# Performance work log

Hardware: AMD Instinct MI355X
Metric: run time of the kernel (lower is better)

Reference implementation:

```python
import jax, jax.numpy as jnp
import numpy as np

H = 1024          # hidden_size
V = 50257         # output_size (vocab)
L = 64            # max_length


def setup_inputs() -> dict:
    key = jax.random.key(0)
    ks = jax.random.split(key, 20)
    s = 0.02
    inp = {
        "input": jax.random.randint(ks[0], (1,), 0, V, dtype=jnp.int64) if jax.config.jax_enable_x64 else jax.random.randint(ks[0], (1,), 0, V, dtype=jnp.int32),
        "hidden": jax.random.normal(ks[1], (2, 1, H), dtype=jnp.float32),
        "encoder_output": jax.random.normal(ks[2], (1, 2 * H), dtype=jnp.float32),
        "encoder_outputs": jax.random.normal(ks[3], (L, 2 * H), dtype=jnp.float32),
        # parameters
        "emb": jax.random.normal(ks[4], (V, H), dtype=jnp.float32) * s,
        "attn_W": jax.random.normal(ks[5], (L, 3 * H), dtype=jnp.float32) * s,
        "attn_b": jnp.zeros((L,), dtype=jnp.float32),
        "comb_W": jax.random.normal(ks[6], (H, 3 * H), dtype=jnp.float32) * s,
        "comb_b": jnp.zeros((H,), dtype=jnp.float32),
        "Wih_f": jax.random.normal(ks[7], (3 * H, H), dtype=jnp.float32) * s,
        "Whh_f": jax.random.normal(ks[8], (3 * H, H), dtype=jnp.float32) * s,
        "bih_f": jnp.zeros((3 * H,), dtype=jnp.float32),
        "bhh_f": jnp.zeros((3 * H,), dtype=jnp.float32),
        "Wih_b": jax.random.normal(ks[9], (3 * H, H), dtype=jnp.float32) * s,
        "Whh_b": jax.random.normal(ks[10], (3 * H, H), dtype=jnp.float32) * s,
        "bih_b": jnp.zeros((3 * H,), dtype=jnp.float32),
        "bhh_b": jnp.zeros((3 * H,), dtype=jnp.float32),
        "out_W": jax.random.normal(ks[11], (V, 2 * H), dtype=jnp.float32) * s,
        "out_b": jnp.zeros((V,), dtype=jnp.float32),
    }
    return inp


def _gru_cell(x, h, Wih, Whh, bih, bhh):
    # PyTorch GRUCell gate math; x, h: (1, H)
    gi = x @ Wih.T + bih                      # (1, 3H)
    gh = h @ Whh.T + bhh                      # (1, 3H)
    ir, iz, inn = jnp.split(gi, 3, axis=1)
    hr, hz, hn = jnp.split(gh, 3, axis=1)
    r = jax.nn.sigmoid(ir + hr)
    z = jax.nn.sigmoid(iz + hz)
    n = jnp.tanh(inn + r * hn)
    return (1.0 - z) * n + z * h


def reference(input, hidden, encoder_output, encoder_outputs,
              emb, attn_W, attn_b, comb_W, comb_b,
              Wih_f, Whh_f, bih_f, bhh_f,
              Wih_b, Whh_b, bih_b, bhh_b,
              out_W, out_b):
    embedded = emb[input]                     # (1, H); dropout is identity in eval
    h0, h1 = hidden[0], hidden[1]             # (1, H) each
    cat3 = jnp.concatenate([embedded, h0, h1], axis=1)          # (1, 3H)
    attn_weights = jax.nn.softmax(cat3 @ attn_W.T + attn_b, axis=1)  # (1, L)
    attn_applied = attn_weights @ encoder_outputs               # (1, 2H)
    comb = jnp.concatenate([embedded, attn_applied], axis=1)    # (1, 3H)
    x = jax.nn.relu(comb @ comb_W.T + comb_b)                   # (1, H)
    hf = _gru_cell(x, h0, Wih_f, Whh_f, bih_f, bhh_f)           # forward dir
    hb = _gru_cell(x, h1, Wih_b, Whh_b, bih_b, bhh_b)           # backward dir (seq_len=1)
    gru_out = jnp.concatenate([hf, hb], axis=1)                 # (1, 2H)
    new_hidden = jnp.stack([hf, hb], axis=0)                    # (2, 1, H)
    log_probs = jax.nn.log_softmax(gru_out @ out_W.T + out_b, axis=1)  # (1, V)
    return (log_probs, new_hidden, attn_weights)
```

## Files before the change

### kernel.cpp

```cpp
#include <hip/hip_runtime.h>
#include <hip/hip_bf16.h>
#include <math.h>

#define H   1024
#define V   50257
#define L   64
#define H2  2048
#define H3  3072

typedef float float4v __attribute__((ext_vector_type(4)));

#define WS_ATTN_LOGITS 0
#define WS_AA          128
#define WS_X           2176
#define WS_GRU         3200
#define WS_LOGITS      5248
#define WS_RED         55552

#define GEMV_BLOCKS 1024
#define GEMV_WAVES  (GEMV_BLOCKS * 4)
#define VC          20480

__device__ inline float waveReduceSum(float v) {
#pragma unroll
    for (int off = 32; off > 0; off >>= 1) v += __shfl_down(v, off, 64);
    return v;
}
__device__ inline float waveAllMax(float v) {
#pragma unroll
    for (int off = 32; off > 0; off >>= 1) v = fmaxf(v, __shfl_xor(v, off, 64));
    return v;
}
__device__ inline float waveAllSum(float v) {
#pragma unroll
    for (int off = 32; off > 0; off >>= 1) v += __shfl_xor(v, off, 64);
    return v;
}
__device__ inline void lse_combine(float& m, float& s, float m2, float s2) {
    float M = fmaxf(m, m2);
    s = s * expf(m - M) + s2 * expf(m2 - M);
    m = M;
}

__global__ __launch_bounds__(256) void k_attn_logits(
        const int* __restrict__ tok_p, const float* __restrict__ hidden,
        const float* __restrict__ emb, const float* __restrict__ attn_W,
        const float* __restrict__ attn_b, float* __restrict__ ws) {
    int b = blockIdx.x;
    int tid = threadIdx.x;
    int tok = tok_p[0];
    const float4* w4   = (const float4*)(attn_W + (size_t)b * H3);
    const float4* emb4 = (const float4*)(emb + (size_t)tok * H);
    const float4* hid4 = (const float4*)hidden;
    float acc = 0.f;
#pragma unroll
    for (int k = 0; k < 3; ++k) {
        int idx = tid + k * 256;
        float4 c = (idx < 256) ? emb4[idx] : hid4[idx - 256];
        float4 w = w4[idx];
        acc += c.x * w.x + c.y * w.y + c.z * w.z + c.w * w.w;
    }
    __shared__ float red[4];
    float p = waveReduceSum(acc);
    int lane = tid & 63, wid = tid >> 6;
    if (lane == 0) red[wid] = p;
    __syncthreads();
    if (tid == 0) ws[WS_ATTN_LOGITS + b] = red[0] + red[1] + red[2] + red[3] + attn_b[b];
}

__global__ __launch_bounds__(256) void k_softmax_applied(
        const float* __restrict__ eo, float* __restrict__ ws,
        float* __restrict__ d_out) {
    __shared__ float aw[64];
    int tid = threadIdx.x;
    if (tid < 64) {
        float x = ws[WS_ATTN_LOGITS + tid];
        float m = waveAllMax(x);
        float e = expf(x - m);
        float s = waveAllSum(e);
        float w = e / s;
        aw[tid] = w;
        if (blockIdx.x == 0) d_out[V + H2 + tid] = w;
    }
    __syncthreads();
    int j = blockIdx.x * 256 + tid;
    float acc = 0.f;
#pragma unroll 8
    for (int l = 0; l < L; ++l) acc += aw[l] * eo[l * H2 + j];
    ws[WS_AA + j] = acc;
}

__global__ __launch_bounds__(256) void k_comb_relu(
        const int* __restrict__ tok_p, const float* __restrict__ emb,
        const float* __restrict__ comb_W, const float* __restrict__ comb_b,
        float* __restrict__ ws) {
    int tid = threadIdx.x;
    int lane = tid & 63, wid = tid >> 6;
    int r = blockIdx.x * 4 + wid;
    int tok = tok_p[0];
    const float4* emb4 = (const float4*)(emb + (size_t)tok * H);
    const float4* aa4  = (const float4*)(ws + WS_AA);
    const float4v* w4  = (const float4v*)(comb_W + (size_t)r * H3);
    float acc = 0.f;
#pragma unroll
    for (int k = 0; k < 12; ++k) {
        int idx = lane + k * 64;
        float4 c = (idx < 256) ? emb4[idx] : aa4[idx - 256];
        float4v w = __builtin_nontemporal_load(&w4[idx]);
        acc += c.x * w.x + c.y * w.y + c.z * w.z + c.w * w.w;
    }
    acc = waveReduceSum(acc);
    if (lane == 0) ws[WS_X + r] = fmaxf(acc + comb_b[r], 0.f);
}

__global__ __launch_bounds__(256) void k_gru(
        const float* __restrict__ hidden,
        const float* __restrict__ Wih_f, const float* __restrict__ Whh_f,
        const float* __restrict__ bih_f, const float* __restrict__ bhh_f,
        const float* __restrict__ Wih_b, const float* __restrict__ Whh_b,
        const float* __restrict__ bih_b, const float* __restrict__ bhh_b,
        float* __restrict__ d_out, float* __restrict__ ws) {
    int tid = threadIdx.x;
    int lane = tid & 63, wid = tid >> 6;
    int w = blockIdx.x * 4 + wid;
    int dir = w >> 10;
    int i = w & (H - 1);
    const float* Wih = dir ? Wih_b : Wih_f;
    const float* Whh = dir ? Whh_b : Whh_f;
    const float* bih = dir ? bih_b : bih_f;
    const float* bhh = dir ? bhh_b : bhh_f;
    const float* h = hidden + dir * H;
    const float4* x4  = (const float4*)(ws + WS_X);
    const float4* h4  = (const float4*)h;
    const float4v* wi0 = (const float4v*)(Wih + (size_t)i * H);
    const float4v* wi1 = (const float4v*)(Wih + (size_t)(H + i) * H);
    const float4v* wi2 = (const float4v*)(Wih + (size_t)(2 * H + i) * H);
    const float4v* wh0 = (const float4v*)(Whh + (size_t)i * H);
    const float4v* wh1 = (const float4v*)(Whh + (size_t)(H + i) * H);
    const float4v* wh2 = (const float4v*)(Whh + (size_t)(2 * H + i) * H);
    float a0 = 0, a1 = 0, a2 = 0, b0 = 0, b1 = 0, b2 = 0;
#pragma unroll
    for (int k = 0; k < 4; ++k) {
        int idx = lane + k * 64;
        float4 xv = x4[idx], hv = h4[idx];
        float4v u0 = __builtin_nontemporal_load(&wi0[idx]);
        float4v u1 = __builtin_nontemporal_load(&wi1[idx]);
        float4v u2 = __builtin_nontemporal_load(&wi2[idx]);
        float4v v0 = __builtin_nontemporal_load(&wh0[idx]);
        float4v v1 = __builtin_nontemporal_load(&wh1[idx]);
        float4v v2 = __builtin_nontemporal_load(&wh2[idx]);
        a0 += xv.x*u0.x + xv.y*u0.y + xv.z*u0.z + xv.w*u0.w;
        a1 += xv.x*u1.x + xv.y*u1.y + xv.z*u1.z + xv.w*u1.w;
        a2 += xv.x*u2.x + xv.y*u2.y + xv.z*u2.z + xv.w*u2.w;
        b0 += hv.x*v0.x + hv.y*v0.y + hv.z*v0.z + hv.w*v0.w;
        b1 += hv.x*v1.x + hv.y*v1.y + hv.z*v1.z + hv.w*v1.w;
        b2 += hv.x*v2.x + hv.y*v2.y + hv.z*v2.z + hv.w*v2.w;
    }
    a0 = waveReduceSum(a0); a1 = waveReduceSum(a1); a2 = waveReduceSum(a2);
    b0 = waveReduceSum(b0); b1 = waveReduceSum(b1); b2 = waveReduceSum(b2);
    if (lane == 0) {
        float ir = a0 + bih[i],     iz = a1 + bih[H + i], in_ = a2 + bih[2 * H + i];
        float hr = b0 + bhh[i],     hz = b1 + bhh[H + i], hn  = b2 + bhh[2 * H + i];
        float r = 1.f / (1.f + expf(-(ir + hr)));
        float z = 1.f / (1.f + expf(-(iz + hz)));
        float n = tanhf(in_ + r * hn);
        float hv = (1.f - z) * n + z * h[i];
        d_out[V + dir * H + i] = hv;
        ws[WS_GRU + dir * H + i] = hv;
    }
}

template <bool NT>
__device__ inline float dot_row(const float4v* __restrict__ w4,
                                const float4 g[8], int lane) {
    float acc = 0.f;
#pragma unroll
    for (int k = 0; k < 8; ++k) {
        int idx = lane + k * 64;
        float4v w = NT ? __builtin_nontemporal_load(&w4[idx]) : w4[idx];
        acc += g[k].x * w.x + g[k].y * w.y + g[k].z * w.z + g[k].w * w.w;
    }
    return acc;
}

__global__ __launch_bounds__(256) void k_gemv_lse(
        const float* __restrict__ out_W, const float* __restrict__ out_b,
        float* __restrict__ ws) {
    int tid = threadIdx.x;
    int lane = tid & 63, wid = tid >> 6;
    int gw = blockIdx.x * 4 + wid;
    const float4* g4 = (const float4*)(ws + WS_GRU);
    float4 g[8];
#pragma unroll
    for (int k = 0; k < 8; ++k) g[k] = g4[lane + k * 64];
    float m = -3.0e38f, s = 0.f;
    for (int v = gw; v < V; v += 2 * GEMV_WAVES) {
        int v2 = v + GEMV_WAVES;
        const float4v* w0 = (const float4v*)(out_W + (size_t)v * H2);
        float acc0, acc1 = 0.f;
        acc0 = (v < VC) ? dot_row<false>(w0, g, lane)
                        : dot_row<true >(w0, g, lane);
        if (v2 < V) {
            const float4v* w1 = (const float4v*)(out_W + (size_t)v2 * H2);
            acc1 = (v2 < VC) ? dot_row<false>(w1, g, lane)
                             : dot_row<true >(w1, g, lane);
        }
        acc0 = waveReduceSum(acc0);
        acc1 = waveReduceSum(acc1);
        if (lane == 0) {
            float logit = acc0 + out_b[v];
            ws[WS_LOGITS + v] = logit;
            float M = fmaxf(m, logit);
            s = s * expf(m - M) + expf(logit - M);
            m = M;
            if (v2 < V) {
                float logit2 = acc1 + out_b[v2];
                ws[WS_LOGITS + v2] = logit2;
                M = fmaxf(m, logit2);
                s = s * expf(m - M) + expf(logit2 - M);
                m = M;
            }
        }
    }
    __shared__ float mm[4], ss[4];
    if (lane == 0) { mm[wid] = m; ss[wid] = s; }
    __syncthreads();
    if (tid == 0) {
        float M = mm[0], S = ss[0];
        lse_combine(M, S, mm[1], ss[1]);
        lse_combine(M, S, mm[2], ss[2]);
        lse_combine(M, S, mm[3], ss[3]);
        ws[WS_RED + 2 * blockIdx.x]     = M;
        ws[WS_RED + 2 * blockIdx.x + 1] = S;
    }
}

__global__ __launch_bounds__(256) void k_lse_sub(const float* __restrict__ ws,
                                                 float* __restrict__ d_out) {
    int tid = threadIdx.x;
    int lane = tid & 63, wid = tid >> 6;
    float m = -3.0e38f, s = 0.f;
#pragma unroll
    for (int k = 0; k < 4; ++k) {
        int i = tid + k * 256;
        lse_combine(m, s, ws[WS_RED + 2 * i], ws[WS_RED + 2 * i + 1]);
    }
#pragma unroll
    for (int off = 32; off > 0; off >>= 1) {
        float m2 = __shfl_xor(m, off, 64);
        float s2 = __shfl_xor(s, off, 64);
        lse_combine(m, s, m2, s2);
    }
    __shared__ float mm[4], ss[4], Csh;
    if (lane == 0) { mm[wid] = m; ss[wid] = s; }
    __syncthreads();
    if (tid == 0) {
        float M = mm[0], S = ss[0];
        lse_combine(M, S, mm[1], ss[1]);
        lse_combine(M, S, mm[2], ss[2]);
        lse_combine(M, S, mm[3], ss[3]);
        Csh = M + logf(S);
    }
    __syncthreads();
    float C = Csh;
    int v = blockIdx.x * 256 + tid;
    if (v < V) d_out[v] = ws[WS_LOGITS + v] - C;
}

extern "C" void kernel_launch(void* const* d_in, const int* in_sizes, int n_in,
                              void* d_out, int out_size, void* d_ws, size_t ws_size,
                              hipStream_t stream) {
    const int*   tok     = (const int*)  d_in[0];
    const float* hidden  = (const float*)d_in[1];
    const float* enc_outs= (const float*)d_in[3];
    const float* emb     = (const float*)d_in[4];
    const float* attn_W  = (const float*)d_in[5];
    const float* attn_b  = (const float*)d_in[6];
    const float* comb_W  = (const float*)d_in[7];
    const float* comb_b  = (const float*)d_in[8];
    const float* Wih_f   = (const float*)d_in[9];
    const float* Whh_f   = (const float*)d_in[10];
    const float* bih_f   = (const float*)d_in[11];
    const float* bhh_f   = (const float*)d_in[12];
    const float* Wih_b   = (const float*)d_in[13];
    const float* Whh_b   = (const float*)d_in[14];
    const float* bih_b   = (const float*)d_in[15];
    const float* bhh_b   = (const float*)d_in[16];
    const float* out_W   = (const float*)d_in[17];
    const float* out_b   = (const float*)d_in[18];
    float* out = (float*)d_out;
    float* ws  = (float*)d_ws;

    hipLaunchKernelGGL(k_attn_logits, dim3(64), dim3(256), 0, stream,
                       tok, hidden, emb, attn_W, attn_b, ws);
    hipLaunchKernelGGL(k_softmax_applied, dim3(8), dim3(256), 0, stream,
                       enc_outs, ws, out);
    hipLaunchKernelGGL(k_comb_relu, dim3(256), dim3(256), 0, stream,
                       tok, emb, comb_W, comb_b, ws);
    hipLaunchKernelGGL(k_gru, dim3(512), dim3(256), 0, stream,
                       hidden, Wih_f, Whh_f, bih_f, bhh_f,
                       Wih_b, Whh_b, bih_b, bhh_b, out, ws);
    hipLaunchKernelGGL(k_gemv_lse, dim3(GEMV_BLOCKS), dim3(256), 0, stream,
                       out_W, out_b, ws);
    hipLaunchKernelGGL(k_lse_sub, dim3(197), dim3(256), 0, stream, ws, out);
}
```

Baseline: 113.9 us.

## Fuse attention logits and softmax-apply kernels; reload GRU vector per row in GEMV

Merges the attention-logit kernel and the softmax/apply kernel into one 8-block kernel. Each block recomputes all 64 attention logits from a shared-memory copy of the concatenated input, removing one launch and the workspace round trip. The price is 8x redundant work on the small attn_W matrix (768 KB), spread over only 8 blocks. Separately, the output GEMV now reloads the GRU vector from memory for every row instead of keeping it in registers. That lowers register pressure but adds cache traffic.

```diff
diff --git a/kernel.cpp b/kernel.cpp
--- a/kernel.cpp
+++ b/kernel.cpp
@@ -10,7 +10,6 @@
 
 typedef float float4v __attribute__((ext_vector_type(4)));
 
-#define WS_ATTN_LOGITS 0
 #define WS_AA          128
 #define WS_X           2176
 #define WS_GRU         3200
@@ -42,39 +41,43 @@
     m = M;
 }
 
-__global__ __launch_bounds__(256) void k_attn_logits(
+__global__ __launch_bounds__(256) void k_attn_fused(
         const int* __restrict__ tok_p, const float* __restrict__ hidden,
         const float* __restrict__ emb, const float* __restrict__ attn_W,
-        const float* __restrict__ attn_b, float* __restrict__ ws) {
-    int b = blockIdx.x;
-    int tid = threadIdx.x;
+        const float* __restrict__ attn_b, const float* __restrict__ eo,
+        float* __restrict__ ws, float* __restrict__ d_out) {
+    __shared__ float c3[H3];
+    __shared__ float lgt[64];
+    __shared__ float aw[64];
+    int tid = threadIdx.x;
+    int lane = tid & 63, wid = tid >> 6;
     int tok = tok_p[0];
-    const float4* w4   = (const float4*)(attn_W + (size_t)b * H3);
     const float4* emb4 = (const float4*)(emb + (size_t)tok * H);
     const float4* hid4 = (const float4*)hidden;
-    float acc = 0.f;
+    float4* c34 = (float4*)c3;
 #pragma unroll
     for (int k = 0; k < 3; ++k) {
         int idx = tid + k * 256;
-        float4 c = (idx < 256) ? emb4[idx] : hid4[idx - 256];
-        float4 w = w4[idx];
-        acc += c.x * w.x + c.y * w.y + c.z * w.z + c.w * w.w;
-    }
-    __shared__ float red[4];
-    float p = waveReduceSum(acc);
-    int lane = tid & 63, wid = tid >> 6;
-    if (lane == 0) red[wid] = p;
-    __syncthreads();
-    if (tid == 0) ws[WS_ATTN_LOGITS + b] = red[0] + red[1] + red[2] + red[3] + attn_b[b];
-}
-
-__global__ __launch_bounds__(256) void k_softmax_applied(
-        const float* __restrict__ eo, float* __restrict__ ws,
-        float* __restrict__ d_out) {
-    __shared__ float aw[64];
-    int tid = threadIdx.x;
+        c34[idx] = (idx < 256) ? emb4[idx] : hid4[idx - 256];
+    }
+    __syncthreads();
+    for (int rr = 0; rr < 16; ++rr) {
+        int r = wid * 16 + rr;
+        const float4* w4 = (const float4*)(attn_W + (size_t)r * H3);
+        float acc = 0.f;
+#pragma unroll
+        for (int j = 0; j < 12; ++j) {
+            int idx = lane + j * 64;
+            float4 c = c34[idx];
+            float4 w = w4[idx];
+            acc += c.x * w.x + c.y * w.y + c.z * w.z + c.w * w.w;
+        }
+        acc = waveReduceSum(acc);
+        if (lane == 0) lgt[r] = acc + attn_b[r];
+    }
+    __syncthreads();
     if (tid < 64) {
-        float x = ws[WS_ATTN_LOGITS + tid];
+        float x = lgt[tid];
         float m = waveAllMax(x);
         float e = expf(x - m);
         float s = waveAllSum(e);
@@ -172,13 +175,14 @@
 
 template <bool NT>
 __device__ inline float dot_row(const float4v* __restrict__ w4,
-                                const float4 g[8], int lane) {
+                                const float4* __restrict__ g4, int lane) {
     float acc = 0.f;
 #pragma unroll
     for (int k = 0; k < 8; ++k) {
         int idx = lane + k * 64;
+        float4  g = g4[idx];
         float4v w = NT ? __builtin_nontemporal_load(&w4[idx]) : w4[idx];
-        acc += g[k].x * w.x + g[k].y * w.y + g[k].z * w.z + g[k].w * w.w;
+        acc += g.x * w.x + g.y * w.y + g.z * w.z + g.w * w.w;
     }
     return acc;
 }
@@ -190,20 +194,17 @@
     int lane = tid & 63, wid = tid >> 6;
     int gw = blockIdx.x * 4 + wid;
     const float4* g4 = (const float4*)(ws + WS_GRU);
-    float4 g[8];
-#pragma unroll
-    for (int k = 0; k < 8; ++k) g[k] = g4[lane + k * 64];
     float m = -3.0e38f, s = 0.f;
     for (int v = gw; v < V; v += 2 * GEMV_WAVES) {
         int v2 = v + GEMV_WAVES;
         const float4v* w0 = (const float4v*)(out_W + (size_t)v * H2);
         float acc0, acc1 = 0.f;
-        acc0 = (v < VC) ? dot_row<false>(w0, g, lane)
-                        : dot_row<true >(w0, g, lane);
+        acc0 = (v < VC) ? dot_row<false>(w0, g4, lane)
+                        : dot_row<true >(w0, g4, lane);
         if (v2 < V) {
             const float4v* w1 = (const float4v*)(out_W + (size_t)v2 * H2);
-            acc1 = (v2 < VC) ? dot_row<false>(w1, g, lane)
-                             : dot_row<true >(w1, g, lane);
+            acc1 = (v2 < VC) ? dot_row<false>(w1, g4, lane)
+                             : dot_row<true >(w1, g4, lane);
         }
         acc0 = waveReduceSum(acc0);
         acc1 = waveReduceSum(acc1);
@@ -291,10 +292,8 @@
     float* out = (float*)d_out;
     float* ws  = (float*)d_ws;
 
-    hipLaunchKernelGGL(k_attn_logits, dim3(64), dim3(256), 0, stream,
-                       tok, hidden, emb, attn_W, attn_b, ws);
-    hipLaunchKernelGGL(k_softmax_applied, dim3(8), dim3(256), 0, stream,
-                       enc_outs, ws, out);
+    hipLaunchKernelGGL(k_attn_fused, dim3(8), dim3(256), 0, stream,
+                       tok, hidden, emb, attn_W, attn_b, enc_outs, ws, out);
     hipLaunchKernelGGL(k_comb_relu, dim3(256), dim3(256), 0, stream,
                        tok, emb, comb_W, comb_b, ws);
     hipLaunchKernelGGL(k_gru, dim3(512), dim3(256), 0, stream,
```

After: 141.6 us. +24.4%, slower.
